# Optimization experiments

Measured on AMD Instinct MI355X. Metric: run time of the kernel, lower is better.

The kernel has to match this reference:

```python
import jax, jax.numpy as jnp
import numpy as np

LN_EPS = 1e-12


def _layernorm(x, gamma, beta):
    mu = jnp.mean(x, axis=-1, keepdims=True)
    var = jnp.var(x, axis=-1, keepdims=True)
    return gamma * (x - mu) / jnp.sqrt(var + LN_EPS) + beta


def setup_inputs() -> dict:
    key = jax.random.key(0)
    ks = jax.random.split(key, 8)
    B, N, C, H = 8, 8192, 512, 8
    FFN = 4 * C
    s_attn = 1.0 / np.sqrt(C)
    s_ffn1 = 1.0 / np.sqrt(C)
    s_ffn2 = 1.0 / np.sqrt(FFN)
    return {
        "x": jax.random.normal(ks[0], (B, N, C), jnp.float32),
        "wq": jax.random.normal(ks[1], (C, C), jnp.float32) * s_attn,
        "bq": jnp.zeros((C,), jnp.float32),
        "wk": jax.random.normal(ks[2], (C, C), jnp.float32) * s_attn,
        "bk": jnp.zeros((C,), jnp.float32),
        "wv": jax.random.normal(ks[3], (C, C), jnp.float32) * s_attn,
        "bv": jnp.zeros((C,), jnp.float32),
        "wo": jax.random.normal(ks[4], (C, C), jnp.float32) * s_attn,
        "bo": jnp.zeros((C,), jnp.float32),
        "gamma1": jnp.ones((C,), jnp.float32),
        "beta1": jnp.zeros((C,), jnp.float32),
        "w_fc1": jax.random.normal(ks[5], (C, FFN), jnp.float32) * s_ffn1,
        "b_fc1": jnp.zeros((FFN,), jnp.float32),
        "w_fc2": jax.random.normal(ks[6], (FFN, C), jnp.float32) * s_ffn2,
        "b_fc2": jnp.zeros((C,), jnp.float32),
        "gamma2": jnp.ones((C,), jnp.float32),
        "beta2": jnp.zeros((C,), jnp.float32),
        "window_size": 64,
        "n_head": 8,
    }


def reference(x, wq, bq, wk, bk, wv, bv, wo, bo, gamma1, beta1,
              w_fc1, b_fc1, w_fc2, b_fc2, gamma2, beta2,
              window_size, n_head):
    B, N, C = x.shape
    ws = window_size
    H = n_head
    dh = C // H

    # window partition: [B, N, C] -> [B*N/ws, ws, C]
    xw = x.reshape(B * N // ws, ws, C)
    shortcut = xw

    # windowed multi-head self-attention
    q = (xw @ wq + bq).reshape(-1, ws, H, dh)
    k = (xw @ wk + bk).reshape(-1, ws, H, dh)
    v = (xw @ wv + bv).reshape(-1, ws, H, dh)
    scale = 1.0 / jnp.sqrt(jnp.asarray(dh, xw.dtype))
    attn = jnp.einsum('wqhd,wkhd->whqk', q, k) * scale  # [nw, H, ws, ws]
    attn = jax.nn.softmax(attn, axis=-1)
    out = jnp.einsum('whqk,wkhd->wqhd', attn, v).reshape(-1, ws, C)
    out = out @ wo + bo

    # residual + LN1
    h = _layernorm(out + shortcut, gamma1, beta1)

    # MLP (fc1 -> GELU -> fc2), residual + LN2
    ff = jax.nn.gelu(h @ w_fc1 + b_fc1, approximate=False) @ w_fc2 + b_fc2
    h = _layernorm(ff + h, gamma2, beta2)

    # window reverse: -> [B, N, C]
    return h.reshape(B, N, C)
```

## Files before the change

### kernel.cpp

```cpp
#include <hip/hip_runtime.h>
#include <hip/hip_bf16.h>

typedef __attribute__((ext_vector_type(8))) short bf16x8;
typedef __attribute__((ext_vector_type(4))) float f32x4;

__device__ __forceinline__ short f2b(float f) {
  return __builtin_bit_cast(short, __float2bfloat16(f));
}
__device__ __forceinline__ float b2f(short s) {
  unsigned u = ((unsigned)(unsigned short)s) << 16;
  return __builtin_bit_cast(float, u);
}

__device__ __forceinline__ void gload16(const void* g, void* l) {
  __builtin_amdgcn_global_load_lds(
      (const __attribute__((address_space(1))) void*)g,
      (__attribute__((address_space(3))) void*)l, 16, 0, 0);
}

__device__ __forceinline__ float gelu_f(float v) {
  float e = __builtin_amdgcn_exp2f(-2.45537082f * v);
  return v * __builtin_amdgcn_rcpf(1.f + e);
}

__global__ void cvt_bf16_vec(const float* __restrict__ src, short* __restrict__ dst, long n) {
  long i = ((long)blockIdx.x * 256 + threadIdx.x) * 8;
  if (i >= n) return;
  f32x4 a = *(const f32x4*)(src + i);
  f32x4 b = *(const f32x4*)(src + i + 4);
  bf16x8 o;
#pragma unroll
  for (int j = 0; j < 4; j++) o[j] = f2b(a[j]);
#pragma unroll
  for (int j = 0; j < 4; j++) o[j + 4] = f2b(b[j]);
  *(bf16x8*)(dst + i) = o;
}

__global__ void pack_all(const float* __restrict__ wq, const float* __restrict__ wk,
                         const float* __restrict__ wv, const float* __restrict__ wo,
                         const float* __restrict__ wfc1, const float* __restrict__ wfc2,
                         const float* __restrict__ bq, const float* __restrict__ bk,
                         const float* __restrict__ bv,
                         short* __restrict__ WQKVT, short* __restrict__ WOT,
                         short* __restrict__ WFC1T, short* __restrict__ WFC2T,
                         float* __restrict__ BQKV) {
  const int b = blockIdx.x;
  if (b >= 3072) {
    for (int t = threadIdx.x; t < 1536; t += 256)
      BQKV[t] = (t < 512) ? bq[t] : ((t < 1024) ? bk[t - 512] : bv[t - 1024]);
    return;
  }
  __shared__ float tile[32][33];
  const float* src;
  short* dst;
  int K, N, tb;
  if (b < 256)       { src = wq;   dst = WQKVT;              K = 512;  N = 512;  tb = b; }
  else if (b < 512)  { src = wk;   dst = WQKVT + 512 * 512;  K = 512;  N = 512;  tb = b - 256; }
  else if (b < 768)  { src = wv;   dst = WQKVT + 1024 * 512; K = 512;  N = 512;  tb = b - 512; }
  else if (b < 1024) { src = wo;   dst = WOT;                K = 512;  N = 512;  tb = b - 768; }
  else if (b < 2048) { src = wfc1; dst = WFC1T;              K = 512;  N = 2048; tb = b - 1024; }
  else               { src = wfc2; dst = WFC2T;              K = 2048; N = 512;  tb = b - 2048; }
  const int ntx = N >> 5;
  const int n0 = (tb % ntx) * 32, k0 = (tb / ntx) * 32;
  const int j = threadIdx.x & 31, i0 = threadIdx.x >> 5;
#pragma unroll
  for (int r = 0; r < 4; r++) {
    int i = i0 + r * 8;
    tile[i][j] = src[(long)(k0 + i) * N + n0 + j];
  }
  __syncthreads();
#pragma unroll
  for (int r = 0; r < 4; r++) {
    int i = i0 + r * 8;
    dst[(long)(n0 + i) * K + k0 + j] = f2b(tile[j][i]);
  }
}

template <int EPI>
__global__ __launch_bounds__(256, 2) void gemm_bt2(
    const short* __restrict__ A, const short* __restrict__ Bt,
    const float* __restrict__ bias, void* __restrict__ Cout, int K, int ldc, int gxN) {
  __shared__ short lds[3 * 12288];
  const int t = threadIdx.x;
  const int w = t >> 6, lane = t & 63;
  const int lr = lane & 15, lg = lane >> 4;

  const int nwg = gridDim.x;
  const int orig = blockIdx.x;
  const int q = nwg >> 3, r = nwg & 7, xcd = orig & 7, idx = orig >> 3;
  const int swz = (xcd < r ? xcd * (q + 1) : r * (q + 1) + (xcd - r) * q) + idx;
  const long m0 = (long)(swz / gxN) * 128;
  const int n0 = (swz % gxN) * 256;

  const int wm = (w >> 1) * 64, wn = (w & 1) * 128;

  f32x4 acc[4][8];
#pragma unroll
  for (int i = 0; i < 4; i++)
#pragma unroll
    for (int j = 0; j < 8; j++) acc[i][j] = f32x4{0.f, 0.f, 0.f, 0.f};

  const int srow = t >> 2;
  const int schunk = (t & 3) ^ ((t >> 3) & 3);
  const short* Ag = A + (m0 + srow) * (long)K + schunk * 8;
  const short* Bg = Bt + ((long)n0 + srow) * K + schunk * 8;
  const long half = (long)64 * K;

#define STAGE(b, kt)                                       \
  {                                                        \
    short* d = lds + (b) * 12288 + t * 8;                  \
    gload16(Ag + (long)(kt) * 32, d);                      \
    gload16(Ag + half + (long)(kt) * 32, d + 2048);        \
    short* db = d + 4096;                                  \
    gload16(Bg + (long)(kt) * 32, db);                     \
    gload16(Bg + half + (long)(kt) * 32, db + 2048);       \
    gload16(Bg + 2 * half + (long)(kt) * 32, db + 4096);   \
    gload16(Bg + 3 * half + (long)(kt) * 32, db + 6144);   \
  }

  const int xsw = (lg ^ ((lr >> 1) & 3)) * 8;
  const int aoff = (wm + lr) * 32 + xsw;
  const int boff = 4096 + (wn + lr) * 32 + xsw;

#define TILE_WAIT(WN)                                        \
  asm volatile("s_waitcnt vmcnt(" #WN ")" ::: "memory");     \
  __builtin_amdgcn_sched_barrier(0);                         \
  __builtin_amdgcn_s_barrier();                              \
  __builtin_amdgcn_sched_barrier(0);

#define BODY(CB)                                                               \
  {                                                                            \
    const short* Lb = lds + (CB) * 12288;                                      \
    bf16x8 a[4], b[8];                                                         \
    _Pragma("unroll") for (int mi = 0; mi < 4; mi++)                           \
        a[mi] = *(const bf16x8*)(Lb + aoff + mi * 512);                        \
    _Pragma("unroll") for (int nj = 0; nj < 8; nj++)                           \
        b[nj] = *(const bf16x8*)(Lb + boff + nj * 512);                        \
    __builtin_amdgcn_s_setprio(1);                                             \
    _Pragma("unroll") for (int mi = 0; mi < 4; mi++)                           \
        _Pragma("unroll") for (int nj = 0; nj < 8; nj++) acc[mi][nj] =         \
            __builtin_amdgcn_mfma_f32_16x16x32_bf16(a[mi], b[nj], acc[mi][nj], \
                                                    0, 0, 0);                  \
    __builtin_amdgcn_s_setprio(0);                                             \
  }

  const int NKT = K >> 5;
  STAGE(0, 0)
  STAGE(1, 1)

  int cb = 0, sb = 2;
  for (int kt = 0; kt < NKT - 1; ++kt) {
    TILE_WAIT(6)
    if (kt + 2 < NKT) STAGE(sb, kt + 2)
    BODY(cb)
    cb = (cb == 2) ? 0 : cb + 1;
    sb = (sb == 2) ? 0 : sb + 1;
  }
  TILE_WAIT(0)
  BODY(cb)
#undef STAGE
#undef TILE_WAIT
#undef BODY

  float bv[8];
#pragma unroll
  for (int nj = 0; nj < 8; nj++) bv[nj] = bias[n0 + wn + nj * 16 + lr];

#pragma unroll
  for (int mi = 0; mi < 4; mi++)
#pragma unroll
    for (int i = 0; i < 4; i++) {
      const long row = m0 + wm + mi * 16 + lg * 4 + i;
      const long rb = row * ldc + n0 + wn + lr;
      short* p = (short*)Cout + rb;
#pragma unroll
      for (int nj = 0; nj < 8; nj++) p[nj * 16] = f2b(gelu_f(acc[mi][nj][i] + bv[nj]));
    }
}

#define DSR(d, a, OFF) \
  asm volatile("ds_read_b128 %0, %1 offset:" OFF : "=v"(d) : "v"(a))
#define SB __builtin_amdgcn_sched_barrier(0)

template <int EPI>
__global__ __launch_bounds__(512, 1) void gemm256(
    const short* __restrict__ A, const short* __restrict__ Bt,
    const float* __restrict__ bias, const short* __restrict__ resB,
    void* __restrict__ Cout, int K, int ldc, int gxN) {
  extern __shared__ short lds[];
  const int t = threadIdx.x;
  const int lane = t & 63, w = t >> 6;
  const int lr = lane & 15, lg = lane >> 4;
  const int wm = w >> 2, wn = w & 3;

  const int nwg = gridDim.x, orig = blockIdx.x;
  const int q8 = nwg >> 3, r8 = nwg & 7, xcd = orig & 7, idx = orig >> 3;
  const int swz = (xcd < r8 ? xcd * (q8 + 1) : r8 * (q8 + 1) + (xcd - r8) * q8) + idx;
  const long m0 = (long)(swz / gxN) * 256;
  const int n0 = (swz % gxN) * 256;

  f32x4 acc[8][4];
#pragma unroll
  for (int i = 0; i < 8; i++)
#pragma unroll
    for (int j = 0; j < 4; j++) acc[i][j] = f32x4{0.f, 0.f, 0.f, 0.f};

  const int srow = t >> 3;
  const int sch = (t & 7) ^ (srow & 7);
  const short* sA = A + (m0 + srow) * (long)K + sch * 8;
  const short* sB = Bt + ((long)n0 + srow) * K + sch * 8;
  const long r64 = (long)64 * K;

#define STG_A(tt, h)                                                     \
  {                                                                      \
    short* d_ = lds + ((tt) & 1) * 16384 + (h) * 8192 + t * 8;           \
    const short* s_ = sA + (h) * 2 * r64 + (long)(tt) * 64;              \
    gload16(s_, d_);                                                     \
    gload16(s_ + r64, d_ + 4096);                                        \
  }
#define STG_B(tt, h)                                                     \
  {                                                                      \
    short* d_ = lds + 32768 + ((tt) & 1) * 16384 + (h) * 8192 + t * 8;   \
    const short* s_ = sB + (h) * 2 * r64 + (long)(tt) * 64;              \
    gload16(s_, d_);                                                     \
    gload16(s_ + r64, d_ + 4096);                                        \
  }

  const unsigned ldsB = (unsigned)(uintptr_t)lds;
  const unsigned xb0 = (unsigned)((lg ^ (lr & 7)) * 16);
  const unsigned xb1 = (unsigned)(((4 + lg) ^ (lr & 7)) * 16);
  const unsigned aRowB = (unsigned)((wm * 128 + lr) * 128);
  const unsigned bRowB = 65536u + (unsigned)((wn * 64 + lr) * 128);

#define BAR                                  \
  {                                          \
    SB;                                      \
    __builtin_amdgcn_s_barrier();            \
    SB;                                      \
  }
#define LGKM0 asm volatile("s_waitcnt lgkmcnt(0)")

  const int NT = K >> 6;
  STG_A(0, 0) STG_A(0, 1) STG_B(0, 0) STG_B(0, 1) STG_B(1, 0) STG_B(1, 1)
  asm volatile("s_waitcnt vmcnt(4)" ::: "memory");
  BAR

#define MFMA8(AC, A0, A1)                                                      \
  {                                                                            \
    __builtin_amdgcn_s_setprio(1);                                             \
    acc[AC][0] = __builtin_amdgcn_mfma_f32_16x16x32_bf16(A0, b00, acc[AC][0], 0, 0, 0); \
    acc[AC][0] = __builtin_amdgcn_mfma_f32_16x16x32_bf16(A1, b01, acc[AC][0], 0, 0, 0); \
    acc[AC][1] = __builtin_amdgcn_mfma_f32_16x16x32_bf16(A0, b10, acc[AC][1], 0, 0, 0); \
    acc[AC][1] = __builtin_amdgcn_mfma_f32_16x16x32_bf16(A1, b11, acc[AC][1], 0, 0, 0); \
    acc[AC][2] = __builtin_amdgcn_mfma_f32_16x16x32_bf16(A0, b20, acc[AC][2], 0, 0, 0); \
    acc[AC][2] = __builtin_amdgcn_mfma_f32_16x16x32_bf16(A1, b21, acc[AC][2], 0, 0, 0); \
    acc[AC][3] = __builtin_amdgcn_mfma_f32_16x16x32_bf16(A0, b30, acc[AC][3], 0, 0, 0); \
    acc[AC][3] = __builtin_amdgcn_mfma_f32_16x16x32_bf16(A1, b31, acc[AC][3], 0, 0, 0); \
    __builtin_amdgcn_s_setprio(0);                                             \
  }

  for (int tt = 0; tt < NT; ++tt) {
    const unsigned dAb = (unsigned)((tt & 1) * 32768);
    const unsigned aA0 = ldsB + aRowB + xb0 + dAb;
    const unsigned aA1 = ldsB + aRowB + xb1 + dAb;
    const unsigned bA0 = ldsB + bRowB + xb0 + dAb;
    const unsigned bA1 = ldsB + bRowB + xb1 + dAb;
    bf16x8 b00, b01, b10, b11, b20, b21, b30, b31;

    {
      DSR(b00, bA0, "0");    DSR(b01, bA1, "0");
      DSR(b10, bA0, "2048"); DSR(b11, bA1, "2048");
      DSR(b20, bA0, "4096"); DSR(b21, bA1, "4096");
      DSR(b30, bA0, "6144"); DSR(b31, bA1, "6144");
      bf16x8 a00, a01, a10, a11;
      DSR(a00, aA0, "0");    DSR(a01, aA1, "0");
      DSR(a10, aA0, "2048"); DSR(a11, aA1, "2048");
      SB;
      if (tt + 1 < NT) STG_A(tt + 1, 0)
      BAR
      LGKM0; SB;
      MFMA8(0, a00, a01)
      MFMA8(1, a10, a11)
      BAR
    }
    {
      bf16x8 a00, a01, a10, a11;
      DSR(a00, aA0, "4096"); DSR(a01, aA1, "4096");
      DSR(a10, aA0, "6144"); DSR(a11, aA1, "6144");
      SB;
      if (tt + 1 < NT) STG_A(tt + 1, 1)
      BAR
      LGKM0; SB;
      MFMA8(2, a00, a01)
      MFMA8(3, a10, a11)
      BAR
    }
    {
      bf16x8 a00, a01, a10, a11;
      DSR(a00, aA0, "8192");  DSR(a01, aA1, "8192");
      DSR(a10, aA0, "10240"); DSR(a11, aA1, "10240");
      SB;
      if (tt + 2 < NT) STG_B(tt + 2, 0)
      BAR
      LGKM0; SB;
      MFMA8(4, a00, a01)
      MFMA8(5, a10, a11)
      BAR
    }
    {
      bf16x8 a00, a01, a10, a11;
      DSR(a00, aA0, "12288"); DSR(a01, aA1, "12288");
      DSR(a10, aA0, "14336"); DSR(a11, aA1, "14336");
      SB;
      if (tt + 2 < NT) STG_B(tt + 2, 1)
      BAR
      LGKM0; SB;
      MFMA8(6, a00, a01)
      MFMA8(7, a10, a11)
      if (tt + 2 < NT) {
        asm volatile("s_waitcnt vmcnt(4)" ::: "memory");
      } else if (tt + 1 < NT) {
        asm volatile("s_waitcnt vmcnt(0)" ::: "memory");
      }
      BAR
    }
  }
#undef MFMA8
#undef STG_A
#undef STG_B

  float bv[4];
#pragma unroll
  for (int nj = 0; nj < 4; nj++) bv[nj] = bias[n0 + wn * 64 + nj * 16 + lr];

#pragma unroll
  for (int a = 0; a < 8; a++)
#pragma unroll
    for (int i = 0; i < 4; i++) {
      const long row = m0 + wm * 128 + a * 16 + lg * 4 + i;
      const long rb = row * ldc + n0 + wn * 64 + lr;
      short* p = (short*)Cout + rb;
      if (EPI == 0) {
#pragma unroll
        for (int nj = 0; nj < 4; nj++) p[nj * 16] = f2b(acc[a][nj][i] + bv[nj]);
      } else {
        const short* rp = resB + rb;
#pragma unroll
        for (int nj = 0; nj < 4; nj++)
          p[nj * 16] = f2b(acc[a][nj][i] + bv[nj] + b2f(rp[nj * 16]));
      }
    }
}
#undef DSR
#undef SB
#undef BAR
#undef LGKM0

__global__ __launch_bounds__(256, 2) void attn_win(const short* __restrict__ QKV,
                                                   short* __restrict__ AO) {
  __shared__ short Vs[64 * 72];
  __shared__ short Vt[64 * 72];
  __shared__ short Ps[64 * 72];
  const int t = threadIdx.x, w = t >> 6, lane = t & 63;
  const int lr = lane & 15, lg = lane >> 4;
  const long base = (long)blockIdx.x * 64 * 1536;
  const long obase = (long)blockIdx.x * 64 * 512;

  for (int h = 0; h < 8; h++) {
    const int co = h * 64;
#pragma unroll
    for (int it = 0; it < 2; it++) {
      int c = t + it * 256;
      int j = c >> 3, d0 = (c & 7) * 8;
      *(bf16x8*)(Vs + j * 72 + d0) =
          *(const bf16x8*)(QKV + base + (long)j * 1536 + 1024 + co + d0);
    }
    bf16x8 qf[2], kf[4][2];
#pragma unroll
    for (int kb = 0; kb < 2; kb++)
      qf[kb] = *(const bf16x8*)(QKV + base + (long)(w * 16 + lr) * 1536 + co + kb * 32 + lg * 8);
#pragma unroll
    for (int nj = 0; nj < 4; nj++)
#pragma unroll
      for (int kb = 0; kb < 2; kb++)
        kf[nj][kb] = *(const bf16x8*)(QKV + base + (long)(nj * 16 + lr) * 1536 + 512 + co +
                                      kb * 32 + lg * 8);
    __syncthreads();

#pragma unroll
    for (int it2 = 0; it2 < 2; it2++) {
      int d = t & 63;
      int j0 = ((t >> 6) + it2 * 4) * 8;
      bf16x8 tmp;
#pragma unroll
      for (int jj = 0; jj < 8; jj++) tmp[jj] = Vs[(j0 + jj) * 72 + d];
      *(bf16x8*)(Vt + d * 72 + j0) = tmp;
    }

    f32x4 s[4];
#pragma unroll
    for (int nj = 0; nj < 4; nj++) {
      s[nj] = f32x4{0.f, 0.f, 0.f, 0.f};
      s[nj] = __builtin_amdgcn_mfma_f32_16x16x32_bf16(qf[0], kf[nj][0], s[nj], 0, 0, 0);
      s[nj] = __builtin_amdgcn_mfma_f32_16x16x32_bf16(qf[1], kf[nj][1], s[nj], 0, 0, 0);
      s[nj] = s[nj] * 0.125f;
    }

#pragma unroll
    for (int i = 0; i < 4; i++) {
      float mx = fmaxf(fmaxf(s[0][i], s[1][i]), fmaxf(s[2][i], s[3][i]));
#pragma unroll
      for (int off = 1; off < 16; off <<= 1) mx = fmaxf(mx, __shfl_xor(mx, off, 64));
      float sum = 0.f;
#pragma unroll
      for (int nj = 0; nj < 4; nj++) {
        float p = __expf(s[nj][i] - mx);
        s[nj][i] = p;
        sum += p;
      }
#pragma unroll
      for (int off = 1; off < 16; off <<= 1) sum += __shfl_xor(sum, off, 64);
      float inv = 1.f / sum;
#pragma unroll
      for (int nj = 0; nj < 4; nj++) s[nj][i] *= inv;
    }

#pragma unroll
    for (int nj = 0; nj < 4; nj++)
#pragma unroll
      for (int i = 0; i < 4; i++)
        Ps[(w * 16 + lg * 4 + i) * 72 + nj * 16 + lr] = f2b(s[nj][i]);

    __syncthreads();

    bf16x8 pa[2];
#pragma unroll
    for (int kb = 0; kb < 2; kb++)
      pa[kb] = *(const bf16x8*)(Ps + (w * 16 + lr) * 72 + kb * 32 + lg * 8);

    f32x4 o[4];
#pragma unroll
    for (int nb = 0; nb < 4; nb++) o[nb] = f32x4{0.f, 0.f, 0.f, 0.f};
#pragma unroll
    for (int kb = 0; kb < 2; kb++)
#pragma unroll
      for (int nb = 0; nb < 4; nb++) {
        bf16x8 vb = *(const bf16x8*)(Vt + (nb * 16 + lr) * 72 + kb * 32 + lg * 8);
        o[nb] = __builtin_amdgcn_mfma_f32_16x16x32_bf16(pa[kb], vb, o[nb], 0, 0, 0);
      }

#pragma unroll
    for (int nb = 0; nb < 4; nb++)
#pragma unroll
      for (int i = 0; i < 4; i++)
        AO[obase + (long)(w * 16 + lg * 4 + i) * 512 + co + nb * 16 + lr] = f2b(o[nb][i]);
    __syncthreads();
  }
}

template <int INB, int OUTB>
__global__ __launch_bounds__(256, 4) void ln_rows(const float* __restrict__ Yf,
                                                  const short* __restrict__ Yb,
                                                  const float* __restrict__ gamma,
                                                  const float* __restrict__ beta,
                                                  short* __restrict__ Hb,
                                                  float* __restrict__ Of) {
  const int w = threadIdx.x >> 6, lane = threadIdx.x & 63;
  const long row = (long)blockIdx.x * 4 + w;
  float v[8];
  if (INB) {
    bf16x8 x = *(const bf16x8*)(Yb + row * 512 + lane * 8);
#pragma unroll
    for (int j = 0; j < 8; j++) v[j] = b2f(x[j]);
  } else {
    f32x4 a = *(const f32x4*)(Yf + row * 512 + lane * 8);
    f32x4 b = *(const f32x4*)(Yf + row * 512 + lane * 8 + 4);
#pragma unroll
    for (int j = 0; j < 4; j++) { v[j] = a[j]; v[j + 4] = b[j]; }
  }
  float s = 0.f, s2 = 0.f;
#pragma unroll
  for (int j = 0; j < 8; j++) { s += v[j]; s2 += v[j] * v[j]; }
#pragma unroll
  for (int off = 1; off < 64; off <<= 1) {
    s += __shfl_xor(s, off, 64);
    s2 += __shfl_xor(s2, off, 64);
  }
  float mu = s * (1.f / 512.f);
  float var = s2 * (1.f / 512.f) - mu * mu;
  float rstd = rsqrtf(fmaxf(var, 0.f) + 1e-12f);
  const int c0 = lane * 8;
  f32x4 ga = *(const f32x4*)(gamma + c0), gb = *(const f32x4*)(gamma + c0 + 4);
  f32x4 ba = *(const f32x4*)(beta + c0), bb = *(const f32x4*)(beta + c0 + 4);
  if (OUTB) {
    bf16x8 o;
#pragma unroll
    for (int j = 0; j < 4; j++) o[j] = f2b(ga[j] * ((v[j] - mu) * rstd) + ba[j]);
#pragma unroll
    for (int j = 0; j < 4; j++) o[j + 4] = f2b(gb[j] * ((v[j + 4] - mu) * rstd) + bb[j]);
    *(bf16x8*)(Hb + row * 512 + c0) = o;
  } else {
    f32x4 o0, o1;
#pragma unroll
    for (int j = 0; j < 4; j++) o0[j] = ga[j] * ((v[j] - mu) * rstd) + ba[j];
#pragma unroll
    for (int j = 0; j < 4; j++) o1[j] = gb[j] * ((v[j + 4] - mu) * rstd) + bb[j];
    *(f32x4*)(Of + row * 512 + c0) = o0;
    *(f32x4*)(Of + row * 512 + c0 + 4) = o1;
  }
}

extern "C" void kernel_launch(void* const* d_in, const int* in_sizes, int n_in,
                              void* d_out, int out_size, void* d_ws, size_t ws_size,
                              hipStream_t stream) {
  (void)in_sizes; (void)n_in; (void)out_size;
  const float* x = (const float*)d_in[0];
  const float* wq = (const float*)d_in[1];
  const float* bq = (const float*)d_in[2];
  const float* wk = (const float*)d_in[3];
  const float* bk = (const float*)d_in[4];
  const float* wv = (const float*)d_in[5];
  const float* bv = (const float*)d_in[6];
  const float* wo = (const float*)d_in[7];
  const float* bo = (const float*)d_in[8];
  const float* g1 = (const float*)d_in[9];
  const float* be1 = (const float*)d_in[10];
  const float* wfc1 = (const float*)d_in[11];
  const float* bfc1 = (const float*)d_in[12];
  const float* wfc2 = (const float*)d_in[13];
  const float* bfc2 = (const float*)d_in[14];
  const float* g2 = (const float*)d_in[15];
  const float* be2 = (const float*)d_in[16];

  const long T = 65536;
  char* ws = (char*)d_ws;

  short* WQKVT = (short*)(ws);
  short* WOT = WQKVT + 1536 * 512;
  short* WFC1T = WOT + 512 * 512;
  short* WFC2T = WFC1T + 2048 * 512;
  float* BQKV = (float*)(WFC2T + 512 * 2048);
  size_t woff = ((size_t)((char*)(BQKV + 1536) - ws) + 255) & ~(size_t)255;

  size_t avail = (ws_size > woff) ? (ws_size - woff) : 0;
  long Tc = T;
  while (Tc > 256 && (size_t)Tc * 7168 > avail) Tc >>= 1;
  const long nch = T / Tc;

  char* R0 = ws + woff;
  char* R1 = R0 + (size_t)Tc * 4096;
  char* R1b = R1 + (size_t)Tc * 1024;
  char* R2 = R1b + (size_t)Tc * 1024;

  short* QKV = (short*)R0;
  short* Y1b = (short*)R0;
  short* FF1 = (short*)R0;
  short* XB = (short*)R1;
  short* AO = (short*)R1b;
  short* Y2b = (short*)R1b;
  short* H = (short*)R2;

  pack_all<<<3073, 256, 0, stream>>>(wq, wk, wv, wo, wfc1, wfc2, bq, bk, bv,
                                     WQKVT, WOT, WFC1T, WFC2T, BQKV);

  const size_t LDSB = 131072;
  for (long c = 0; c < nch; c++) {
    const long t0 = c * Tc;
    const int mb = (int)(Tc / 256);
    const int mb2 = (int)(Tc / 128);
    cvt_bf16_vec<<<(int)(Tc / 4), 256, 0, stream>>>(x + t0 * 512, XB, Tc * 512);
    gemm256<0><<<mb * 6, 512, LDSB, stream>>>(XB, WQKVT, BQKV, nullptr,
                                              (void*)QKV, 512, 1536, 6);
    attn_win<<<(int)(Tc / 64), 256, 0, stream>>>(QKV, AO);
    gemm256<2><<<mb * 2, 512, LDSB, stream>>>(AO, WOT, bo, XB,
                                              (void*)Y1b, 512, 512, 2);
    ln_rows<1, 1><<<(int)(Tc / 4), 256, 0, stream>>>(nullptr, Y1b, g1, be1, H, nullptr);
    gemm_bt2<1><<<mb2 * 8, 256, 0, stream>>>(H, WFC1T, bfc1, (void*)FF1, 512, 2048, 8);
    gemm256<2><<<mb * 2, 512, LDSB, stream>>>(FF1, WFC2T, bfc2, H,
                                              (void*)Y2b, 2048, 512, 2);
    ln_rows<1, 0><<<(int)(Tc / 4), 256, 0, stream>>>(nullptr, Y2b, g2, be2, nullptr,
                                                     (float*)d_out + t0 * 512);
  }
}
```

Before: 705.6 us.

## Fuse residual add and LayerNorm into full-row out-proj and fc2 GEMMs

Adds a gemm_ln kernel that computes a 128x512 output tile per block, so each block owns complete rows. It adds bias and residual, then reduces row sums across waves through LDS and applies LayerNorm in the epilogue. The separate ln_rows kernels and their bf16 intermediate buffers are removed, which cuts launches and global memory round trips. The trade-off is a new, simpler GEMM main loop with static LDS that may be less efficient than the tuned gemm256, especially for the K=2048 fc2 GEMM.

New measurement: 743.3 us. 5.3% more time.

```diff
diff --git a/kernel.cpp b/kernel.cpp
--- a/kernel.cpp
+++ b/kernel.cpp
@@ -178,6 +178,157 @@
     }
 }
 
+template <int EPI>
+__global__ __launch_bounds__(512, 1) void gemm_ln(
+    const short* __restrict__ A, const short* __restrict__ Bt,
+    const float* __restrict__ bias, const short* __restrict__ res,
+    const float* __restrict__ gamma, const float* __restrict__ beta,
+    void* __restrict__ Cout, int K) {
+  __shared__ short lds[3 * 20480];
+  const int t = threadIdx.x;
+  const int w = t >> 6, lane = t & 63;
+  const int lr = lane & 15, lg = lane >> 4;
+  const int wm = (w >> 2) * 64, wn = (w & 3) * 128;
+
+  const int nwg = gridDim.x;
+  const int orig = blockIdx.x;
+  const int q = nwg >> 3, r = nwg & 7, xcd = orig & 7, idx = orig >> 3;
+  const int swz = (xcd < r ? xcd * (q + 1) : r * (q + 1) + (xcd - r) * q) + idx;
+  const long m0 = (long)swz * 128;
+
+  f32x4 acc[4][8];
+#pragma unroll
+  for (int i = 0; i < 4; i++)
+#pragma unroll
+    for (int j = 0; j < 8; j++) acc[i][j] = f32x4{0.f, 0.f, 0.f, 0.f};
+
+  const int srow = t >> 2;
+  const int schunk = (t & 3) ^ ((t >> 3) & 3);
+  const short* Ag = A + (m0 + srow) * (long)K + schunk * 8;
+  const short* Bg = Bt + (long)srow * K + schunk * 8;
+  const long q128 = (long)128 * K;
+
+#define STAGE(b, kt)                                        \
+  {                                                         \
+    short* d = lds + (b) * 20480 + t * 8;                   \
+    gload16(Ag + (long)(kt) * 32, d);                       \
+    short* db = d + 4096;                                   \
+    gload16(Bg + (long)(kt) * 32, db);                      \
+    gload16(Bg + q128 + (long)(kt) * 32, db + 4096);        \
+    gload16(Bg + 2 * q128 + (long)(kt) * 32, db + 8192);    \
+    gload16(Bg + 3 * q128 + (long)(kt) * 32, db + 12288);   \
+  }
+
+  const int xsw = (lg ^ ((lr >> 1) & 3)) * 8;
+  const int aoff = (wm + lr) * 32 + xsw;
+  const int boff = 4096 + (wn + lr) * 32 + xsw;
+
+#define TILE_WAIT(WN)                                        \
+  asm volatile("s_waitcnt vmcnt(" #WN ")" ::: "memory");     \
+  __builtin_amdgcn_sched_barrier(0);                         \
+  __builtin_amdgcn_s_barrier();                              \
+  __builtin_amdgcn_sched_barrier(0);
+
+#define BODY(CB)                                                               \
+  {                                                                            \
+    const short* Lb = lds + (CB) * 20480;                                      \
+    bf16x8 a[4], b[8];                                                         \
+    _Pragma("unroll") for (int mi = 0; mi < 4; mi++)                           \
+        a[mi] = *(const bf16x8*)(Lb + aoff + mi * 512);                        \
+    _Pragma("unroll") for (int nj = 0; nj < 8; nj++)                           \
+        b[nj] = *(const bf16x8*)(Lb + boff + nj * 512);                        \
+    __builtin_amdgcn_s_setprio(1);                                             \
+    _Pragma("unroll") for (int mi = 0; mi < 4; mi++)                           \
+        _Pragma("unroll") for (int nj = 0; nj < 8; nj++) acc[mi][nj] =         \
+            __builtin_amdgcn_mfma_f32_16x16x32_bf16(a[mi], b[nj], acc[mi][nj], \
+                                                    0, 0, 0);                  \
+    __builtin_amdgcn_s_setprio(0);                                             \
+  }
+
+  const int NKT = K >> 5;
+  STAGE(0, 0)
+  STAGE(1, 1)
+
+  int cb = 0, sb = 2;
+  for (int kt = 0; kt < NKT - 1; ++kt) {
+    TILE_WAIT(5)
+    if (kt + 2 < NKT) STAGE(sb, kt + 2)
+    BODY(cb)
+    cb = (cb == 2) ? 0 : cb + 1;
+    sb = (sb == 2) ? 0 : sb + 1;
+  }
+  TILE_WAIT(0)
+  BODY(cb)
+#undef STAGE
+#undef TILE_WAIT
+#undef BODY
+
+  float bvv[8], gv[8], btv[8];
+#pragma unroll
+  for (int nj = 0; nj < 8; nj++) {
+    int col = wn + nj * 16 + lr;
+    bvv[nj] = bias[col];
+    gv[nj] = gamma[col];
+    btv[nj] = beta[col];
+  }
+
+  __syncthreads();
+  float* sums = (float*)lds;
+
+#pragma unroll
+  for (int mi = 0; mi < 4; mi++)
+#pragma unroll
+    for (int i = 0; i < 4; i++) {
+      const int row = wm + mi * 16 + lg * 4 + i;
+      const long rb = (m0 + row) * 512 + wn + lr;
+      const short* rp = res + rb;
+      float s = 0.f, s2 = 0.f;
+#pragma unroll
+      for (int nj = 0; nj < 8; nj++) {
+        float v = acc[mi][nj][i] + bvv[nj] + b2f(rp[nj * 16]);
+        acc[mi][nj][i] = v;
+        s += v;
+        s2 += v * v;
+      }
+#pragma unroll
+      for (int off = 1; off < 16; off <<= 1) {
+        s += __shfl_xor(s, off, 64);
+        s2 += __shfl_xor(s2, off, 64);
+      }
+      if (lr == 0) {
+        float* p = sums + (row * 4 + (w & 3)) * 2;
+        p[0] = s;
+        p[1] = s2;
+      }
+    }
+  __syncthreads();
+
+#pragma unroll
+  for (int mi = 0; mi < 4; mi++)
+#pragma unroll
+    for (int i = 0; i < 4; i++) {
+      const int row = wm + mi * 16 + lg * 4 + i;
+      const float* p = sums + row * 8;
+      float S = p[0] + p[2] + p[4] + p[6];
+      float S2 = p[1] + p[3] + p[5] + p[7];
+      float mu = S * (1.f / 512.f);
+      float var = S2 * (1.f / 512.f) - mu * mu;
+      float rstd = rsqrtf(fmaxf(var, 0.f) + 1e-12f);
+      const long rb = (m0 + row) * 512 + wn + lr;
+      if (EPI == 0) {
+        short* o = (short*)Cout + rb;
+#pragma unroll
+        for (int nj = 0; nj < 8; nj++)
+          o[nj * 16] = f2b(gv[nj] * ((acc[mi][nj][i] - mu) * rstd) + btv[nj]);
+      } else {
+        float* o = (float*)Cout + rb;
+#pragma unroll
+        for (int nj = 0; nj < 8; nj++)
+          o[nj * 16] = gv[nj] * ((acc[mi][nj][i] - mu) * rstd) + btv[nj];
+      }
+    }
+}
+
 #define DSR(d, a, OFF) \
   asm volatile("ds_read_b128 %0, %1 offset:" OFF : "=v"(d) : "v"(a))
 #define SB __builtin_amdgcn_sched_barrier(0)
@@ -455,58 +606,6 @@
       for (int i = 0; i < 4; i++)
         AO[obase + (long)(w * 16 + lg * 4 + i) * 512 + co + nb * 16 + lr] = f2b(o[nb][i]);
     __syncthreads();
-  }
-}
-
-template <int INB, int OUTB>
-__global__ __launch_bounds__(256, 4) void ln_rows(const float* __restrict__ Yf,
-                                                  const short* __restrict__ Yb,
-                                                  const float* __restrict__ gamma,
-                                                  const float* __restrict__ beta,
-                                                  short* __restrict__ Hb,
-                                                  float* __restrict__ Of) {
-  const int w = threadIdx.x >> 6, lane = threadIdx.x & 63;
-  const long row = (long)blockIdx.x * 4 + w;
-  float v[8];
-  if (INB) {
-    bf16x8 x = *(const bf16x8*)(Yb + row * 512 + lane * 8);
-#pragma unroll
-    for (int j = 0; j < 8; j++) v[j] = b2f(x[j]);
-  } else {
-    f32x4 a = *(const f32x4*)(Yf + row * 512 + lane * 8);
-    f32x4 b = *(const f32x4*)(Yf + row * 512 + lane * 8 + 4);
-#pragma unroll
-    for (int j = 0; j < 4; j++) { v[j] = a[j]; v[j + 4] = b[j]; }
-  }
-  float s = 0.f, s2 = 0.f;
-#pragma unroll
-  for (int j = 0; j < 8; j++) { s += v[j]; s2 += v[j] * v[j]; }
-#pragma unroll
-  for (int off = 1; off < 64; off <<= 1) {
-    s += __shfl_xor(s, off, 64);
-    s2 += __shfl_xor(s2, off, 64);
-  }
-  float mu = s * (1.f / 512.f);
-  float var = s2 * (1.f / 512.f) - mu * mu;
-  float rstd = rsqrtf(fmaxf(var, 0.f) + 1e-12f);
-  const int c0 = lane * 8;
-  f32x4 ga = *(const f32x4*)(gamma + c0), gb = *(const f32x4*)(gamma + c0 + 4);
-  f32x4 ba = *(const f32x4*)(beta + c0), bb = *(const f32x4*)(beta + c0 + 4);
-  if (OUTB) {
-    bf16x8 o;
-#pragma unroll
-    for (int j = 0; j < 4; j++) o[j] = f2b(ga[j] * ((v[j] - mu) * rstd) + ba[j]);
-#pragma unroll
-    for (int j = 0; j < 4; j++) o[j + 4] = f2b(gb[j] * ((v[j + 4] - mu) * rstd) + bb[j]);
-    *(bf16x8*)(Hb + row * 512 + c0) = o;
-  } else {
-    f32x4 o0, o1;
-#pragma unroll
-    for (int j = 0; j < 4; j++) o0[j] = ga[j] * ((v[j] - mu) * rstd) + ba[j];
-#pragma unroll
-    for (int j = 0; j < 4; j++) o1[j] = gb[j] * ((v[j + 4] - mu) * rstd) + bb[j];
-    *(f32x4*)(Of + row * 512 + c0) = o0;
-    *(f32x4*)(Of + row * 512 + c0 + 4) = o1;
   }
 }
 
@@ -553,11 +652,9 @@
   char* R2 = R1b + (size_t)Tc * 1024;
 
   short* QKV = (short*)R0;
-  short* Y1b = (short*)R0;
   short* FF1 = (short*)R0;
   short* XB = (short*)R1;
   short* AO = (short*)R1b;
-  short* Y2b = (short*)R1b;
   short* H = (short*)R2;
 
   pack_all<<<3073, 256, 0, stream>>>(wq, wk, wv, wo, wfc1, wfc2, bq, bk, bv,
@@ -572,13 +669,9 @@
     gemm256<0><<<mb * 6, 512, LDSB, stream>>>(XB, WQKVT, BQKV, nullptr,
                                               (void*)QKV, 512, 1536, 6);
     attn_win<<<(int)(Tc / 64), 256, 0, stream>>>(QKV, AO);
-    gemm256<2><<<mb * 2, 512, LDSB, stream>>>(AO, WOT, bo, XB,
-                                              (void*)Y1b, 512, 512, 2);
-    ln_rows<1, 1><<<(int)(Tc / 4), 256, 0, stream>>>(nullptr, Y1b, g1, be1, H, nullptr);
+    gemm_ln<0><<<mb2, 512, 0, stream>>>(AO, WOT, bo, XB, g1, be1, (void*)H, 512);
     gemm_bt2<1><<<mb2 * 8, 256, 0, stream>>>(H, WFC1T, bfc1, (void*)FF1, 512, 2048, 8);
-    gemm256<2><<<mb * 2, 512, LDSB, stream>>>(FF1, WFC2T, bfc2, H,
-                                              (void*)Y2b, 2048, 512, 2);
-    ln_rows<1, 0><<<(int)(Tc / 4), 256, 0, stream>>>(nullptr, Y2b, g2, be2, nullptr,
-                                                     (float*)d_out + t0 * 512);
-  }
-}
+    gemm_ln<1><<<mb2, 512, 0, stream>>>(FF1, WFC2T, bfc2, H, g2, be2,
+                                        (void*)((float*)d_out + t0 * 512), 2048);
+  }
+}
```
